# Kernel tuning notes

Hardware: AMD Instinct MI355X
Metric: run time of the kernel (lower is better)

Reference implementation:

```python
import jax, jax.numpy as jnp
import numpy as np

IN_F, OUT_F = 4096, 4096
IGS, OGS = 8, 1          # in_group_size, out_group_size
NCB, CBS = 1, 65536      # num_codebooks, codebook_size (2**16)
NIG, NOG = IN_F // IGS, OUT_F // OGS


def setup_inputs() -> dict:
    key = jax.random.key(0)
    k1, k2, k3, k4, k5 = jax.random.split(key, 5)
    x = jax.random.normal(k1, (4, 2048, IN_F), jnp.float32)
    codes = jax.random.randint(k2, (NOG, NIG, NCB), 0, CBS, dtype=jnp.int32)
    codebooks = jax.random.normal(k3, (NCB, CBS, OGS, IGS), jnp.float32) * 0.05
    scales = jax.random.uniform(k4, (NOG, 1, 1, 1), jnp.float32, 0.5, 1.5)
    bias = jax.random.normal(k5, (OUT_F,), jnp.float32) * 0.01
    return {"x": x, "codes": codes, "codebooks": codebooks, "scales": scales, "bias": bias}


def _dequantize_weight(codes, codebooks, scales):
    # codes: [nog, nig, ncb] int; codebooks: [ncb, cbs, ogs, igs]
    ncb, cbs, ogs, igs = codebooks.shape
    nog, nig, _ = codes.shape
    flat = codebooks.reshape(ncb, cbs, ogs * igs)
    # embedding_bag(mode='sum'): gather each codebook's vector and sum over codebooks
    gathered = flat[jnp.arange(ncb)[None, None, :], codes]  # [nog, nig, ncb, ogs*igs]
    w = gathered.sum(axis=2).reshape(nog, nig, ogs, igs)
    w = w * scales  # scales broadcasts over [nog, nig, ogs, igs]
    # [nog, nig, ogs, igs] -> [nog, ogs, nig, igs] -> [out_features, in_features]
    return w.swapaxes(1, 2).reshape(nog * ogs, nig * igs)


def reference(x, codes, codebooks, scales, bias):
    W = _dequantize_weight(codes, codebooks, scales)  # [OUT_F, IN_F]
    return x @ W.T + bias
```

## Files before the change

### kernel.cpp

```cpp
#include <hip/hip_runtime.h>
#include <hip/hip_bf16.h>

#define M_DIM 8192
#define N_DIM 4096
#define K_DIM 4096
#define NOG 4096
#define NIG 512

typedef __bf16 bf16x8 __attribute__((ext_vector_type(8)));
typedef float f32x4 __attribute__((ext_vector_type(4)));
typedef short short8 __attribute__((ext_vector_type(8)));

typedef const __attribute__((address_space(1))) void* as1_cvoid_p;
typedef __attribute__((address_space(3))) void* as3_void_p;

__device__ __forceinline__ unsigned short f2bf(float f) {
  union { float f; unsigned u; } c; c.f = f;
  unsigned u = c.u;
  return (unsigned short)((u + 0x7fffu + ((u >> 16) & 1u)) >> 16);
}

__global__ __launch_bounds__(256) void cvt_x_kernel(const float* __restrict__ x,
                                                    unsigned short* __restrict__ xb,
                                                    int n8) {
  int i = blockIdx.x * blockDim.x + threadIdx.x;
  int stride = gridDim.x * blockDim.x;
  for (; i < n8; i += stride) {
    const float4* p = (const float4*)(x) + (size_t)i * 2;
    float4 a = p[0], b = p[1];
    short8 o;
    o[0] = (short)f2bf(a.x); o[1] = (short)f2bf(a.y);
    o[2] = (short)f2bf(a.z); o[3] = (short)f2bf(a.w);
    o[4] = (short)f2bf(b.x); o[5] = (short)f2bf(b.y);
    o[6] = (short)f2bf(b.z); o[7] = (short)f2bf(b.w);
    ((short8*)xb)[i] = o;
  }
}

__global__ __launch_bounds__(256) void dequant_kernel(const int* __restrict__ codes,
                                                      const float* __restrict__ cb,
                                                      unsigned short* __restrict__ wb) {
  int idx = blockIdx.x * blockDim.x + threadIdx.x;
  int code = codes[idx];
  const float4* p = (const float4*)(cb + (size_t)code * 8);
  float4 a = p[0], b = p[1];
  short8 o;
  o[0] = (short)f2bf(a.x); o[1] = (short)f2bf(a.y);
  o[2] = (short)f2bf(a.z); o[3] = (short)f2bf(a.w);
  o[4] = (short)f2bf(b.x); o[5] = (short)f2bf(b.y);
  o[6] = (short)f2bf(b.z); o[7] = (short)f2bf(b.w);
  ((short8*)wb)[idx] = o;
}


#define BAR() __builtin_amdgcn_s_barrier()
#define WAITLGKM() asm volatile("s_waitcnt lgkmcnt(0)" ::: "memory")
#define PRIO1() __builtin_amdgcn_s_setprio(1)
#define PRIO0() __builtin_amdgcn_s_setprio(0)

#define STAGE_A(slot_, h_, kt_) do { \
  _Pragma("unroll") for (int i_ = 0; i_ < 2; ++i_) { \
    const unsigned short* src_ = Ag + (size_t)(sa_roff[i_] + (h_) * 64) * 4096 + (unsigned)((kt_) + sa_koff[i_]); \
    __builtin_amdgcn_global_load_lds((as1_cvoid_p)src_, \
      (as3_void_p)(smem + (slot_) * 32768 + sa_lds[i_] + (h_) * 4096), 16, 0, 0); \
  } } while (0)

#define STAGE_B(slot_, h_, kt_) do { \
  _Pragma("unroll") for (int i_ = 0; i_ < 2; ++i_) { \
    const unsigned short* src_ = Bg + (size_t)(sb_roff[i_] + (h_) * 32) * 4096 + (unsigned)((kt_) + sb_koff[i_]); \
    __builtin_amdgcn_global_load_lds((as1_cvoid_p)src_, \
      (as3_void_p)(smem + 65536 + (slot_) * 32768 + sb_lds[i_] + (h_) * 2048), 16, 0, 0); \
  } } while (0)

#define LDA(ma_, slot_) \
  _Pragma("unroll") for (int m_ = 0; m_ < 4; ++m_) \
  _Pragma("unroll") for (int kk_ = 0; kk_ < 2; ++kk_) \
    af[m_][kk_] = *(const bf16x8*)(smem + (slot_) * 32768 + aRd + ((ma_) * 4 + m_) * 1024 + kk_ * 16384);

#define LDB(n0_, dst_, slot_) \
  _Pragma("unroll") for (int n_ = 0; n_ < 2; ++n_) \
  _Pragma("unroll") for (int kk_ = 0; kk_ < 2; ++kk_) \
    dst_[n_][kk_] = *(const bf16x8*)(smem + (slot_) * 32768 + bRd + ((n0_) + n_) * 1024 + kk_ * 16384);

#define MM(m0_, nb_, bfr_) \
  _Pragma("unroll") for (int m_ = 0; m_ < 4; ++m_) \
  _Pragma("unroll") for (int n_ = 0; n_ < 2; ++n_) \
  _Pragma("unroll") for (int kk_ = 0; kk_ < 2; ++kk_) \
    acc[(m0_) + m_][(nb_) + n_] = __builtin_amdgcn_mfma_f32_16x16x32_bf16( \
        af[m_][kk_], bfr_[n_][kk_], acc[(m0_) + m_][(nb_) + n_], 0, 0, 0);

#define GROUP(SLOT_, MODE_, KT_) do { \
   \
  LDA(0, SLOT_); LDB(0, bf0, SLOT_); \
  if ((MODE_) >= 1) STAGE_A((SLOT_) ^ 1, 1, (KT_) + 64); \
  BAR(); WAITLGKM(); PRIO1(); MM(0, 0, bf0); PRIO0(); BAR(); \
   \
  LDB(2, bf1, SLOT_); \
  if ((MODE_) == 2) STAGE_A(SLOT_, 0, (KT_) + 128); \
  BAR(); WAITLGKM(); PRIO1(); MM(0, 2, bf1); PRIO0(); BAR(); \
   \
  LDA(1, SLOT_); \
  if ((MODE_) == 2) STAGE_B(SLOT_, 0, (KT_) + 128); \
  BAR(); WAITLGKM(); PRIO1(); MM(4, 0, bf0); PRIO0(); BAR(); \
   \
  if ((MODE_) == 2) STAGE_B(SLOT_, 1, (KT_) + 128); \
  if ((MODE_) == 2) { asm volatile("s_waitcnt vmcnt(6)" ::: "memory"); } \
  else if ((MODE_) == 1) { asm volatile("s_waitcnt vmcnt(0)" ::: "memory"); } \
  BAR(); PRIO1(); MM(4, 2, bf1); PRIO0(); BAR(); \
} while (0)

__global__ __launch_bounds__(512) void gemm8_kernel(
    const unsigned short* __restrict__ A,
    const unsigned short* __restrict__ B,
    const float* __restrict__ scales,
    const float* __restrict__ bias,
    float* __restrict__ C) {
  extern __shared__ char smem[];

  const int bid = blockIdx.x;
  const int swz = (bid & 7) * 64 + (bid >> 3);
  const int bm = swz >> 4;
  const int bn = swz & 15;

  const int tid = threadIdx.x;
  const int w = tid >> 6;
  const int l = tid & 63;
  const int wr = w >> 2;
  const int wcol = w & 3;

  const int llog = l ^ (((l >> 5) & 1) << 1);
  int sa_roff[2], sa_koff[2], sa_lds[2];
  int sb_roff[2], sb_koff[2], sb_lds[2];
#pragma unroll
  for (int i = 0; i < 2; ++i) {
    int u = w * 2 + i;
    int panel = u >> 3;
    int rbA = (u >> 2) & 1, chA = u & 3;
    sa_roff[i] = rbA * 128 + chA * 16 + (llog >> 2);
    sa_koff[i] = panel * 32 + (llog & 3) * 8;
    sa_lds[i] = panel * 16384 + rbA * 8192 + chA * 1024;
    int bb = (u >> 1) & 3, hk = u & 1;
    sb_roff[i] = bb * 64 + hk * 16 + (llog >> 2);
    sb_koff[i] = panel * 32 + (llog & 3) * 8;
    sb_lds[i] = panel * 16384 + bb * 4096 + hk * 1024;
  }

  const unsigned short* Ag = A + (size_t)bm * 256 * 4096;
  const unsigned short* Bg = B + (size_t)bn * 256 * 4096;

  const int xr = ((l >> 4) * 16) ^ (((l >> 3) & 1) << 5);
  const int aRd = (wr * 128 + (l & 15)) * 64 + xr;
  const int bRd = 65536 + (wcol * 64 + (l & 15)) * 64 + xr;

  f32x4 acc[8][4];
#pragma unroll
  for (int m = 0; m < 8; ++m)
#pragma unroll
    for (int n = 0; n < 4; ++n) acc[m][n] = (f32x4){0.f, 0.f, 0.f, 0.f};

  bf16x8 af[4][2], bf0[2][2], bf1[2][2];

  STAGE_A(0, 0, 0); STAGE_A(0, 1, 0); STAGE_B(0, 0, 0); STAGE_B(0, 1, 0);
  asm volatile("s_waitcnt vmcnt(4)" ::: "memory");
  STAGE_A(1, 0, 64); STAGE_B(1, 0, 64); STAGE_B(1, 1, 64);
  asm volatile("s_waitcnt vmcnt(6)" ::: "memory");
  BAR();

  int kt = 0;
  for (int j = 0; j < 31; ++j) {
    GROUP(0, 2, kt);
    GROUP(1, 2, kt + 64);
    kt += 128;
  }
  GROUP(0, 1, kt);
  GROUP(1, 0, kt + 64);

  const int row0 = bm * 256 + wr * 128 + ((l >> 4) << 2);
  const int col0 = bn * 256 + wcol * 64 + (l & 15);
#pragma unroll
  for (int n = 0; n < 4; ++n) {
    const int col = col0 + n * 16;
    const float s = scales[col];
    const float bv = bias[col];
#pragma unroll
    for (int m = 0; m < 8; ++m) {
      f32x4 v = acc[m][n];
      const int r = row0 + m * 16;
#pragma unroll
      for (int j = 0; j < 4; ++j)
        C[(size_t)(r + j) * 4096 + col] = v[j] * s + bv;
    }
  }
}

extern "C" void kernel_launch(void* const* d_in, const int* in_sizes, int n_in,
                              void* d_out, int out_size, void* d_ws, size_t ws_size,
                              hipStream_t stream) {
  const float* x = (const float*)d_in[0];
  const int* codes = (const int*)d_in[1];
  const float* cb = (const float*)d_in[2];
  const float* scales = (const float*)d_in[3];
  const float* bias = (const float*)d_in[4];
  float* out = (float*)d_out;

  unsigned short* xb = (unsigned short*)d_ws;
  unsigned short* wb = (unsigned short*)((char*)d_ws + (size_t)M_DIM * K_DIM * 2);

  hipFuncSetAttribute((const void*)gemm8_kernel,
                      hipFuncAttributeMaxDynamicSharedMemorySize, 131072);

  cvt_x_kernel<<<4096, 256, 0, stream>>>(x, xb, (M_DIM * K_DIM) / 8);
  dequant_kernel<<<(NOG * NIG) / 256, 256, 0, stream>>>(codes, cb, wb);
  gemm8_kernel<<<dim3((M_DIM / 256) * (N_DIM / 256)), 512, 131072, stream>>>(
      xb, wb, scales, bias, out);
}
```

Measured before the change: 271.2 us.

## Split GEMM phases into quarter-MFMA blocks with partial LDS waits and fewer barriers

Restructures the software pipeline of the bf16 MFMA GEMM main loop. LDS fragment reads are split into halves so MFMAs can start after partial lgkmcnt waits. The next slot's first B fragment is prefetched across the group boundary. Barriers per group drop from eight to four, with vmcnt waits retuned to match the new global->LDS staging order. This trades fewer stalls for tighter, more fragile dependency counting, and a wrong vmcnt or lgkmcnt value would race on LDS.

```diff
diff --git a/kernel.cpp b/kernel.cpp
--- a/kernel.cpp
+++ b/kernel.cpp
@@ -54,9 +54,11 @@
 
 
 #define BAR() __builtin_amdgcn_s_barrier()
-#define WAITLGKM() asm volatile("s_waitcnt lgkmcnt(0)" ::: "memory")
+#define SB() __builtin_amdgcn_sched_barrier(0)
 #define PRIO1() __builtin_amdgcn_s_setprio(1)
 #define PRIO0() __builtin_amdgcn_s_setprio(0)
+#define LGKM(N_) asm volatile("s_waitcnt lgkmcnt(" #N_ ")" ::: "memory")
+#define VMC(N_) asm volatile("s_waitcnt vmcnt(" #N_ ")" ::: "memory")
 
 #define STAGE_A(slot_, h_, kt_) do { \
   _Pragma("unroll") for (int i_ = 0; i_ < 2; ++i_) { \
@@ -72,41 +74,47 @@
       (as3_void_p)(smem + 65536 + (slot_) * 32768 + sb_lds[i_] + (h_) * 2048), 16, 0, 0); \
   } } while (0)
 
-#define LDA(ma_, slot_) \
-  _Pragma("unroll") for (int m_ = 0; m_ < 4; ++m_) \
+#define LDA_Q(q_, ma_, slot_) \
+  _Pragma("unroll") for (int j_ = 0; j_ < 2; ++j_) \
   _Pragma("unroll") for (int kk_ = 0; kk_ < 2; ++kk_) \
-    af[m_][kk_] = *(const bf16x8*)(smem + (slot_) * 32768 + aRd + ((ma_) * 4 + m_) * 1024 + kk_ * 16384);
+    af[(q_) * 2 + j_][kk_] = *(const bf16x8*)(smem + (slot_) * 32768 + aRd + ((ma_) * 4 + (q_) * 2 + j_) * 1024 + kk_ * 16384);
 
 #define LDB(n0_, dst_, slot_) \
   _Pragma("unroll") for (int n_ = 0; n_ < 2; ++n_) \
   _Pragma("unroll") for (int kk_ = 0; kk_ < 2; ++kk_) \
     dst_[n_][kk_] = *(const bf16x8*)(smem + (slot_) * 32768 + bRd + ((n0_) + n_) * 1024 + kk_ * 16384);
 
-#define MM(m0_, nb_, bfr_) \
-  _Pragma("unroll") for (int m_ = 0; m_ < 4; ++m_) \
+#define MM_Q(base_, q_, nb_, bfr_) \
+  _Pragma("unroll") for (int j_ = 0; j_ < 2; ++j_) \
   _Pragma("unroll") for (int n_ = 0; n_ < 2; ++n_) \
   _Pragma("unroll") for (int kk_ = 0; kk_ < 2; ++kk_) \
-    acc[(m0_) + m_][(nb_) + n_] = __builtin_amdgcn_mfma_f32_16x16x32_bf16( \
-        af[m_][kk_], bfr_[n_][kk_], acc[(m0_) + m_][(nb_) + n_], 0, 0, 0);
+    acc[(base_) + (q_) * 2 + j_][(nb_) + n_] = __builtin_amdgcn_mfma_f32_16x16x32_bf16( \
+        af[(q_) * 2 + j_][kk_], bfr_[n_][kk_], acc[(base_) + (q_) * 2 + j_][(nb_) + n_], 0, 0, 0);
 
 #define GROUP(SLOT_, MODE_, KT_) do { \
    \
-  LDA(0, SLOT_); LDB(0, bf0, SLOT_); \
+  LDA_Q(0, 0, SLOT_); LDA_Q(1, 0, SLOT_); LDB(2, bf1, SLOT_); \
   if ((MODE_) >= 1) STAGE_A((SLOT_) ^ 1, 1, (KT_) + 64); \
-  BAR(); WAITLGKM(); PRIO1(); MM(0, 0, bf0); PRIO0(); BAR(); \
-   \
-  LDB(2, bf1, SLOT_); \
+  LGKM(8); SB(); PRIO1(); MM_Q(0, 0, 0, bf0); \
+  LGKM(4); SB(); MM_Q(0, 1, 0, bf0); PRIO0(); \
+  if ((MODE_) >= 1) { VMC(8); } else { VMC(0); } \
+  BAR(); \
+   \
   if ((MODE_) == 2) STAGE_A(SLOT_, 0, (KT_) + 128); \
-  BAR(); WAITLGKM(); PRIO1(); MM(0, 2, bf1); PRIO0(); BAR(); \
-   \
-  LDA(1, SLOT_); \
+  PRIO1(); MM_Q(0, 0, 2, bf1); MM_Q(0, 1, 2, bf1); PRIO0(); \
+  if ((MODE_) == 2) { VMC(8); } else if ((MODE_) == 1) { VMC(6); } \
+  BAR(); \
+   \
+  LDA_Q(0, 1, SLOT_); LDA_Q(1, 1, SLOT_); \
   if ((MODE_) == 2) STAGE_B(SLOT_, 0, (KT_) + 128); \
-  BAR(); WAITLGKM(); PRIO1(); MM(4, 0, bf0); PRIO0(); BAR(); \
-   \
+  LGKM(4); SB(); PRIO1(); MM_Q(4, 0, 0, bf0); \
+  LGKM(0); SB(); MM_Q(4, 1, 0, bf0); PRIO0(); \
+  if ((MODE_) == 2) { VMC(6); } else if ((MODE_) == 1) { VMC(2); } \
+  BAR(); \
+   \
+  if ((MODE_) >= 1) { LDB(0, bf0, (SLOT_) ^ 1); } \
   if ((MODE_) == 2) STAGE_B(SLOT_, 1, (KT_) + 128); \
-  if ((MODE_) == 2) { asm volatile("s_waitcnt vmcnt(6)" ::: "memory"); } \
-  else if ((MODE_) == 1) { asm volatile("s_waitcnt vmcnt(0)" ::: "memory"); } \
-  BAR(); PRIO1(); MM(4, 2, bf1); PRIO0(); BAR(); \
+  PRIO1(); MM_Q(4, 0, 2, bf1); MM_Q(4, 1, 2, bf1); PRIO0(); \
 } while (0)
 
 __global__ __launch_bounds__(512) void gemm8_kernel(
@@ -160,11 +168,12 @@
 
   bf16x8 af[4][2], bf0[2][2], bf1[2][2];
 
-  STAGE_A(0, 0, 0); STAGE_A(0, 1, 0); STAGE_B(0, 0, 0); STAGE_B(0, 1, 0);
-  asm volatile("s_waitcnt vmcnt(4)" ::: "memory");
+  STAGE_A(0, 0, 0); STAGE_B(0, 0, 0); STAGE_B(0, 1, 0);
+  STAGE_A(0, 1, 0);
   STAGE_A(1, 0, 64); STAGE_B(1, 0, 64); STAGE_B(1, 1, 64);
-  asm volatile("s_waitcnt vmcnt(6)" ::: "memory");
+  VMC(8);
   BAR();
+  LDB(0, bf0, 0);
 
   int kt = 0;
   for (int j = 0; j < 31; ++j) {
```

Result: faster. 262.9 us (-3.1%).
